# Performance work log

Measured on AMD Instinct MI355X. Metric: run time of the kernel, lower is better.

Reference implementation:

```python
import jax, jax.numpy as jnp
import numpy as np

C = 512
NH = 8
GROUPS = 32
EPS = 1e-5


def setup_inputs() -> dict:
    key = jax.random.key(0)
    ks = jax.random.split(key, 7)
    B, T, H, W = 4, 24, 32, 32
    x = jax.random.normal(ks[0], (B, C, T, H, W), dtype=jnp.float32)
    gn_w = jnp.ones((C,), jnp.float32)
    gn_b = jnp.zeros((C,), jnp.float32)
    # 1x1 Conv1d weights stored as [out_ch, in_ch] (kernel dim of size 1 dropped)
    qkv_w = jax.random.normal(ks[1], (3 * C, C), dtype=jnp.float32) / np.sqrt(C)
    qkv_b = jax.random.normal(ks[2], (3 * C,), dtype=jnp.float32) * 0.02
    proj_w = jax.random.normal(ks[3], (C, C), dtype=jnp.float32) / np.sqrt(C)
    proj_b = jax.random.normal(ks[4], (C,), dtype=jnp.float32) * 0.02
    return {"x": x, "gn_w": gn_w, "gn_b": gn_b, "qkv_w": qkv_w,
            "qkv_b": qkv_b, "proj_w": proj_w, "proj_b": proj_b}


def reference(x, gn_w, gn_b, qkv_w, qkv_b, proj_w, proj_b):
    B, Cc, T, H, W = x.shape
    hd = Cc // NH
    # [B,C,T,H,W] -> [B*H*W, C, T]
    xf = jnp.transpose(x, (0, 3, 4, 1, 2)).reshape(B * H * W, Cc, T)
    # GroupNorm over (C/G, T) per group
    xg = xf.reshape(-1, GROUPS, Cc // GROUPS, T)
    mean = xg.mean(axis=(2, 3), keepdims=True)
    var = xg.var(axis=(2, 3), keepdims=True)
    xn = ((xg - mean) * jax.lax.rsqrt(var + EPS)).reshape(-1, Cc, T)
    xn = xn * gn_w[:, None] + gn_b[:, None]
    # 1x1 conv QKV: [n, 3C, T]
    qkv = jnp.einsum('nct,dc->ndt', xn, qkv_w) + qkv_b[:, None]
    qkv = qkv.reshape(-1, 3, NH, hd, T)
    q, k, v = qkv[:, 0], qkv[:, 1], qkv[:, 2]  # each [n, h, d, T]
    scale = 1.0 / np.sqrt(hd)
    attn = jax.nn.softmax(jnp.einsum('nhdt,nhds->nhts', q, k) * scale, axis=-1)
    out = jnp.einsum('nhts,nhds->nhtd', attn, v)        # [n, h, T, d]
    out = out.transpose(0, 2, 1, 3).reshape(-1, T, Cc)   # [n, T, C]
    out = out.transpose(0, 2, 1)                         # [n, C, T]
    out = jnp.einsum('nct,dc->ndt', out, proj_w) + proj_b[:, None]
    out = out.reshape(B, H, W, Cc, T).transpose(0, 3, 4, 1, 2)
    return x + out
```

## Files before the change

### kernel.cpp

```cpp
#include <hip/hip_runtime.h>
#include <hip/hip_bf16.h>
#include <stdint.h>

#define C_    512
#define T_    24
#define HWSZ  1024
#define NN    4096
#define JTOT  98304
#define EPSV  1e-5f

typedef short short8 __attribute__((ext_vector_type(8)));
typedef short short4v __attribute__((ext_vector_type(4)));
typedef float f32x4 __attribute__((ext_vector_type(4)));
typedef float f32x2 __attribute__((ext_vector_type(2)));
typedef __bf16 bf16x2 __attribute__((ext_vector_type(2)));

typedef __attribute__((address_space(1))) const uint32_t glob_u32;
typedef __attribute__((address_space(3))) uint32_t lds_u32;

#if __has_builtin(__builtin_amdgcn_fdot2_f32_bf16)
#define HAS_DOT2 1
#else
#define HAS_DOT2 0
#endif

__device__ __forceinline__ unsigned short f2bf(float f) {
  union { float f; unsigned u; } v; v.f = f;
  unsigned r = v.u + 0x7fffu + ((v.u >> 16) & 1u);
  return (unsigned short)(r >> 16);
}
__device__ __forceinline__ float bf2f(unsigned short b) {
  union { unsigned u; float f; } v; v.u = ((unsigned)b) << 16;
  return v.f;
}
__device__ __forceinline__ float bflo(uint32_t u) {
  union { unsigned u; float f; } v; v.u = u << 16; return v.f;
}
__device__ __forceinline__ float bfhi(uint32_t u) {
  union { unsigned u; float f; } v; v.u = u & 0xffff0000u; return v.f;
}
__device__ __forceinline__ uint32_t pkbf(float a, float b) {
  return (uint32_t)f2bf(a) | ((uint32_t)f2bf(b) << 16);
}
__device__ __forceinline__ bf16x2 asbf2(uint32_t u) {
  union { uint32_t u; bf16x2 v; } c; c.u = u; return c.v;
}

__device__ __forceinline__ void gload_lds16(const void* g, void* l) {
  __builtin_amdgcn_global_load_lds((glob_u32*)g, (lds_u32*)l, 16, 0, 0);
}

__global__ void k_cvt(const float* __restrict__ qkvw, const float* __restrict__ projw,
                      unsigned short* __restrict__ qkvw_bf, unsigned short* __restrict__ projw_bf) {
  int i = blockIdx.x * 256 + threadIdx.x;
  if (i < 786432) qkvw_bf[i] = f2bf(qkvw[i]);
  if (i < 262144) projw_bf[i] = f2bf(projw[i]);
}

__global__ __launch_bounds__(256) void k_stats(const float* __restrict__ x,
                                               float* __restrict__ mean, float* __restrict__ rstd) {
  int bid = blockIdx.x;
  int g = bid & 31, hwt = (bid >> 5) & 15, b = bid >> 9;
  int tid = threadIdx.x, lane = tid & 63, grp = tid >> 6;
  int hw = hwt * 64 + lane;
  float s = 0.f, sq = 0.f;
  for (int ct = grp; ct < 384; ct += 4) {
    int c = g * 16 + ct / 24;
    int t = ct % 24;
    float v = x[((size_t)((b * 512 + c) * 24 + t) << 10) + hw];
    s += v; sq += v * v;
  }
  __shared__ float ls[4][64], lq[4][64];
  ls[grp][lane] = s; lq[grp][lane] = sq;
  __syncthreads();
  if (tid < 64) {
    float S = ls[0][tid] + ls[1][tid] + ls[2][tid] + ls[3][tid];
    float Q = lq[0][tid] + lq[1][tid] + lq[2][tid] + lq[3][tid];
    float m = S * (1.f / 384.f);
    float var = Q * (1.f / 384.f) - m * m;
    int n = b * HWSZ + hwt * 64 + tid;
    mean[n * 32 + g] = m;
    rstd[n * 32 + g] = rsqrtf(var + EPSV);
  }
}

__global__ __launch_bounds__(256) void k_norm(const float* __restrict__ x,
                                              const float* __restrict__ mean, const float* __restrict__ rstd,
                                              const float* __restrict__ gnw, const float* __restrict__ gnb,
                                              unsigned short* __restrict__ xn) {
  __shared__ unsigned short xs[64][260];
  const int bid = blockIdx.x;
  const int hwt = bid & 15;
  const int chalf = (bid >> 4) & 1;
  const int tb = bid >> 5;
  const int t = tb % 24, b = tb / 24;
  const int hw0 = hwt * 64;
  const int tid = threadIdx.x;
  const int w = tid >> 6, lane = tid & 63;

  const int cslot = w * 4 + (lane >> 4);
  const int hwr = (lane & 15) * 4;
#pragma unroll
  for (int k = 0; k < 8; ++k) {
    const int crel = k * 32 + cslot * 2;
    const int c = chalf * 256 + crel;
    const float4 v0 = *reinterpret_cast<const float4*>(
        &x[(((size_t)(b * 512 + c) * 24 + t) << 10) + hw0 + hwr]);
    const float4 v1 = *reinterpret_cast<const float4*>(
        &x[(((size_t)(b * 512 + c + 1) * 24 + t) << 10) + hw0 + hwr]);
    *reinterpret_cast<uint32_t*>(&xs[hwr + 0][crel]) = pkbf(v0.x, v1.x);
    *reinterpret_cast<uint32_t*>(&xs[hwr + 1][crel]) = pkbf(v0.y, v1.y);
    *reinterpret_cast<uint32_t*>(&xs[hwr + 2][crel]) = pkbf(v0.z, v1.z);
    *reinterpret_cast<uint32_t*>(&xs[hwr + 3][crel]) = pkbf(v0.w, v1.w);
  }

  const int crel8 = (lane & 31) * 8;
  const int c8 = chalf * 256 + crel8;
  const int g = c8 >> 4;
  float gw[8], gb[8];
#pragma unroll
  for (int i = 0; i < 8; ++i) { gw[i] = gnw[c8 + i]; gb[i] = gnb[c8 + i]; }
  float mm[8], rr[8];
#pragma unroll
  for (int p = 0; p < 8; ++p) {
    const int nrel = (p * 4 + w) * 2 + (lane >> 5);
    const int ng = b * HWSZ + hw0 + nrel;
    mm[p] = mean[ng * 32 + g];
    rr[p] = rstd[ng * 32 + g];
  }
  __syncthreads();

#pragma unroll
  for (int p = 0; p < 8; ++p) {
    const int nrel = (p * 4 + w) * 2 + (lane >> 5);
    const short4v lo = *reinterpret_cast<const short4v*>(&xs[nrel][crel8]);
    const short4v hi = *reinterpret_cast<const short4v*>(&xs[nrel][crel8 + 4]);
    float y[8];
#pragma unroll
    for (int i = 0; i < 4; ++i) {
      y[i]     = (bf2f((unsigned short)lo[i]) - mm[p]) * rr[p] * gw[i]     + gb[i];
      y[i + 4] = (bf2f((unsigned short)hi[i]) - mm[p]) * rr[p] * gw[i + 4] + gb[i + 4];
    }
    uint4 wv;
    wv.x = pkbf(y[0], y[1]);
    wv.y = pkbf(y[2], y[3]);
    wv.z = pkbf(y[4], y[5]);
    wv.w = pkbf(y[6], y[7]);
    const size_t j = (size_t)t * NN + b * HWSZ + hw0 + nrel;
    *reinterpret_cast<uint4*>(&xn[j * C_ + c8]) = wv;
  }
}

#define STAGE8(mat, half, tile, Gptr, row0)                                           \
  {                                                                                   \
    unsigned short* _l = &lds[(((tile) & 1) * 2 + (mat))][half][(w * 2) * 512];       \
    const unsigned short* _g = (Gptr) +                                               \
        (size_t)((row0) + (half) * 128 + (w * 2) * 8 + srow) * 512 +                  \
        (tile) * 64 + sslot * 8;                                                      \
    gload_lds16(_g, _l);                                                              \
    gload_lds16(_g + 8 * 512, _l + 512);                                              \
  }

__global__ __launch_bounds__(512, 2) void k_gemm8(
    const unsigned short* __restrict__ A,
    const unsigned short* __restrict__ B,
    const float* __restrict__ bias,
    uint32_t* __restrict__ outP) {
  __shared__ __attribute__((aligned(16))) unsigned short lds[4][2][8192];
  const int bid = blockIdx.x;
  const int cpx = 2304 >> 3;
  const int lid = (bid & 7) * cpx + (bid >> 3);
  const int mt = lid % 6, jt = lid / 6;
  const int m0 = mt * 256, j0 = jt * 256;
  const int tid = threadIdx.x;
  const int w = tid >> 6, lane = tid & 63;
  const int l16 = lane & 15, lqq = lane >> 4;
  const int wm = w >> 2, wn = w & 3;
  const int srow = lane >> 3;
  const int sslot = (lane & 7) ^ srow;
  const int k0off = l16 * 64 + ((lqq ^ (l16 & 7)) * 8);
  const int k1off = l16 * 64 + (((lqq + 4) ^ (l16 & 7)) * 8);

  f32x4 acc[8][4];
#pragma unroll
  for (int i = 0; i < 8; ++i)
#pragma unroll
    for (int j = 0; j < 4; ++j) acc[i][j] = {0.f, 0.f, 0.f, 0.f};

  STAGE8(0, 0, 0, A, m0); STAGE8(0, 1, 0, A, m0);
  STAGE8(1, 0, 0, B, j0); STAGE8(1, 1, 0, B, j0);
  STAGE8(0, 0, 1, A, m0); STAGE8(0, 1, 1, A, m0);
  STAGE8(1, 0, 1, B, j0);
  asm volatile("s_waitcnt vmcnt(6)" ::: "memory");
  __builtin_amdgcn_s_barrier();

  for (int t = 0; t < 8; ++t) {
    const int buf = t & 1;
    const unsigned short* Ab = &lds[buf * 2 + 0][wm][0];
    const unsigned short* Bb = &lds[buf * 2 + 1][wn >> 1][(wn & 1) * 4096];
    short8 a[8][2], bb[4][2];
#pragma unroll
    for (int rr = 0; rr < 8; ++rr) {
      a[rr][0] = *reinterpret_cast<const short8*>(Ab + rr * 1024 + k0off);
      a[rr][1] = *reinterpret_cast<const short8*>(Ab + rr * 1024 + k1off);
    }
#pragma unroll
    for (int cc = 0; cc < 2; ++cc) {
      bb[cc][0] = *reinterpret_cast<const short8*>(Bb + cc * 1024 + k0off);
      bb[cc][1] = *reinterpret_cast<const short8*>(Bb + cc * 1024 + k1off);
    }
    if (t < 7) STAGE8(1, 1, t + 1, B, j0);
    asm volatile("" ::: "memory");
    __builtin_amdgcn_s_barrier();
    asm volatile("s_waitcnt lgkmcnt(0)" ::: "memory");
    __builtin_amdgcn_sched_barrier(0);
    __builtin_amdgcn_s_setprio(1);
#pragma unroll
    for (int rr = 0; rr < 4; ++rr)
#pragma unroll
      for (int cc = 0; cc < 2; ++cc) {
        acc[rr][cc] = __builtin_amdgcn_mfma_f32_16x16x32_bf16(a[rr][0], bb[cc][0], acc[rr][cc], 0, 0, 0);
        acc[rr][cc] = __builtin_amdgcn_mfma_f32_16x16x32_bf16(a[rr][1], bb[cc][1], acc[rr][cc], 0, 0, 0);
      }
    __builtin_amdgcn_s_setprio(0);
    asm volatile("" ::: "memory");
    __builtin_amdgcn_s_barrier();
#pragma unroll
    for (int cc = 2; cc < 4; ++cc) {
      bb[cc][0] = *reinterpret_cast<const short8*>(Bb + cc * 1024 + k0off);
      bb[cc][1] = *reinterpret_cast<const short8*>(Bb + cc * 1024 + k1off);
    }
    if (t < 6) STAGE8(0, 0, t + 2, A, m0);
    asm volatile("" ::: "memory");
    __builtin_amdgcn_s_barrier();
    asm volatile("s_waitcnt lgkmcnt(0)" ::: "memory");
    __builtin_amdgcn_sched_barrier(0);
    __builtin_amdgcn_s_setprio(1);
#pragma unroll
    for (int rr = 0; rr < 4; ++rr)
#pragma unroll
      for (int cc = 2; cc < 4; ++cc) {
        acc[rr][cc] = __builtin_amdgcn_mfma_f32_16x16x32_bf16(a[rr][0], bb[cc][0], acc[rr][cc], 0, 0, 0);
        acc[rr][cc] = __builtin_amdgcn_mfma_f32_16x16x32_bf16(a[rr][1], bb[cc][1], acc[rr][cc], 0, 0, 0);
      }
    __builtin_amdgcn_s_setprio(0);
    asm volatile("" ::: "memory");
    __builtin_amdgcn_s_barrier();
    if (t < 6) STAGE8(0, 1, t + 2, A, m0);
    asm volatile("" ::: "memory");
    __builtin_amdgcn_s_barrier();
    __builtin_amdgcn_s_setprio(1);
#pragma unroll
    for (int rr = 4; rr < 8; ++rr)
#pragma unroll
      for (int cc = 0; cc < 2; ++cc) {
        acc[rr][cc] = __builtin_amdgcn_mfma_f32_16x16x32_bf16(a[rr][0], bb[cc][0], acc[rr][cc], 0, 0, 0);
        acc[rr][cc] = __builtin_amdgcn_mfma_f32_16x16x32_bf16(a[rr][1], bb[cc][1], acc[rr][cc], 0, 0, 0);
      }
    __builtin_amdgcn_s_setprio(0);
    asm volatile("" ::: "memory");
    __builtin_amdgcn_s_barrier();
    if (t < 6) STAGE8(1, 0, t + 2, B, j0);
    asm volatile("" ::: "memory");
    __builtin_amdgcn_s_barrier();
    __builtin_amdgcn_s_setprio(1);
#pragma unroll
    for (int rr = 4; rr < 8; ++rr)
#pragma unroll
      for (int cc = 2; cc < 4; ++cc) {
        acc[rr][cc] = __builtin_amdgcn_mfma_f32_16x16x32_bf16(a[rr][0], bb[cc][0], acc[rr][cc], 0, 0, 0);
        acc[rr][cc] = __builtin_amdgcn_mfma_f32_16x16x32_bf16(a[rr][1], bb[cc][1], acc[rr][cc], 0, 0, 0);
      }
    __builtin_amdgcn_s_setprio(0);
    asm volatile("" ::: "memory");
    if (t < 6) {
      asm volatile("s_waitcnt vmcnt(6)" ::: "memory");
    } else if (t == 6) {
      asm volatile("s_waitcnt vmcnt(0)" ::: "memory");
    }
    __builtin_amdgcn_s_barrier();
  }

#pragma unroll
  for (int rr = 0; rr < 8; ++rr) {
#pragma unroll
    for (int cc = 0; cc < 4; ++cc) {
      const int row = m0 + wm * 128 + rr * 16 + lqq * 4;
      const int col = j0 + wn * 64 + cc * 16 + l16;
      const int t_ = col >> 12, n = col & 4095;
      const int mat = row >> 9;
      const int hh = (row >> 6) & 7;
      const int d = row & 63;
      const int ch = d >> 3;
      const int dp = (d & 7) >> 1;
      const size_t base = (size_t)((mat * 8 + hh) * 8 + ch) * 393216;
      uint2 st;
      st.x = pkbf(acc[rr][cc][0] + bias[row], acc[rr][cc][1] + bias[row + 1]);
      st.y = pkbf(acc[rr][cc][2] + bias[row + 2], acc[rr][cc][3] + bias[row + 3]);
      *reinterpret_cast<uint2*>(&outP[base + ((size_t)t_ * 4096 + n) * 4 + dp]) = st;
    }
  }
}

__global__ __launch_bounds__(256, 3) void k_proj(
    const unsigned short* __restrict__ A,
    const unsigned short* __restrict__ B,
    const float* __restrict__ bias,
    const float* __restrict__ xres,
    float* __restrict__ outf) {
  __shared__ __attribute__((aligned(16))) unsigned short As[2][8192];
  const int bid = blockIdx.x;
  const int cpx = 3072 >> 3;
  const int lid = (bid & 7) * cpx + (bid >> 3);
  const int mt = lid & 3, jt = lid >> 2;
  const int m0 = mt * 128, j0 = jt * 128;
  const int tid = threadIdx.x;
  const int w = tid >> 6, lane = tid & 63;
  const int l16 = lane & 15, lqq = lane >> 4;
  const int wm = w >> 1, wn = w & 1;
  const int srow8 = lane >> 3;
  const int sslot = (lane & 7) ^ srow8;
  const int k0off = l16 * 64 + ((lqq ^ (l16 & 7)) * 8);
  const int k1off = l16 * 64 + (((lqq + 4) ^ (l16 & 7)) * 8);

  f32x4 acc[4][4];
#pragma unroll
  for (int i = 0; i < 4; ++i)
#pragma unroll
    for (int j = 0; j < 4; ++j) acc[i][j] = {0.f, 0.f, 0.f, 0.f};

#define PSTAGE(buf, tile)                                                             \
  {                                                                                   \
    _Pragma("unroll")                                                                 \
    for (int m_ = 0; m_ < 4; ++m_) {                                                  \
      unsigned short* _l = &As[buf][m_ * 2048 + w * 512];                             \
      const unsigned short* _g = A +                                                  \
          (size_t)(m0 + m_ * 32 + w * 8 + srow8) * 512 + (tile) * 64 + sslot * 8;     \
      gload_lds16(_g, _l);                                                            \
    }                                                                                 \
  }

#define LOADB(dst, tt)                                                                \
  {                                                                                   \
    _Pragma("unroll")                                                                 \
    for (int cc = 0; cc < 4; ++cc) {                                                  \
      const int jj_ = j0 + wn * 64 + cc * 16 + l16;                                   \
      _Pragma("unroll")                                                               \
      for (int ks = 0; ks < 2; ++ks)                                                  \
        dst[cc][ks] = *reinterpret_cast<const short8*>(                               \
            &B[((size_t)((tt) * 8 + ks * 4 + lqq) * JTOT + jj_) * 8]);                \
    }                                                                                 \
  }

#define PSTEP(t, CUR, NXT)                                                            \
  {                                                                                   \
    if ((t) < 7) { PSTAGE(((t) + 1) & 1, (t) + 1); LOADB(NXT, (t) + 1); }             \
    const unsigned short* Ab = &As[(t) & 1][(wm * 64) * 64];                          \
    _Pragma("unroll")                                                                 \
    for (int rr = 0; rr < 4; ++rr) {                                                  \
      short8 a0 = *reinterpret_cast<const short8*>(Ab + rr * 1024 + k0off);           \
      short8 a1 = *reinterpret_cast<const short8*>(Ab + rr * 1024 + k1off);           \
      _Pragma("unroll")                                                               \
      for (int cc = 0; cc < 4; ++cc) {                                                \
        acc[rr][cc] = __builtin_amdgcn_mfma_f32_16x16x32_bf16(a0, CUR[cc][0], acc[rr][cc], 0, 0, 0); \
        acc[rr][cc] = __builtin_amdgcn_mfma_f32_16x16x32_bf16(a1, CUR[cc][1], acc[rr][cc], 0, 0, 0); \
      }                                                                               \
    }                                                                                 \
    __syncthreads();                                                                  \
  }

  short8 bbA[4][2], bbB[4][2];
  PSTAGE(0, 0);
  LOADB(bbA, 0);
  __syncthreads();

  PSTEP(0, bbA, bbB);
  PSTEP(1, bbB, bbA);
  PSTEP(2, bbA, bbB);
  PSTEP(3, bbB, bbA);
  PSTEP(4, bbA, bbB);
  PSTEP(5, bbB, bbA);
  PSTEP(6, bbA, bbB);
  PSTEP(7, bbB, bbA);

#pragma unroll
  for (int mi = 0; mi < 4; ++mi) {
#pragma unroll
    for (int ni = 0; ni < 4; ++ni) {
      const int dbase = m0 + wm * 64 + mi * 16 + lqq * 4;
      const int jj = j0 + wn * 64 + ni * 16 + l16;
      const int t_ = jj >> 12, n = jj & 4095;
      const int b_ = n >> 10, hw = n & 1023;
#pragma unroll
      for (int r = 0; r < 4; ++r) {
        size_t o = (((size_t)(b_ * 512 + dbase + r) * 24 + t_) << 10) + hw;
        outf[o] = xres[o] + acc[mi][ni][r] + bias[dbase + r];
      }
    }
  }
}

__global__ __launch_bounds__(512) void k_attn(const uint32_t* __restrict__ qkvP,
                                              unsigned short* __restrict__ aoC) {
  __shared__ uint4 kq[2][1536];
  const int ntile = blockIdx.x, h = blockIdx.y;
  const int n0 = ntile * 64;
  const int tid = threadIdx.x;
  const int lane = tid & 63, slot = tid >> 6;
  const int t0 = slot * 3;
  const int BLK = 393216;
  const size_t bQ = (size_t)((0 * 8 + h) * 8) * BLK;
  const size_t bK = (size_t)((1 * 8 + h) * 8) * BLK;
  const size_t bV = (size_t)((2 * 8 + h) * 8) * BLK;
  const int ub = tid & 448;

#define STAGE_M(cbase, dstbuf)                                                        \
  {                                                                                   \
    _Pragma("unroll")                                                                 \
    for (int p = 0; p < 3; ++p) {                                                     \
      const int u = p * 512 + tid;                                                    \
      gload_lds16(qkvP + (cbase) + ((size_t)(u >> 6) * 4096 + n0 + (u & 63)) * 4,     \
                  (void*)(&kq[dstbuf][p * 512 + ub]));                                \
    }                                                                                 \
  }

#define STAGE_QK(c_)                                                                  \
  {                                                                                   \
    STAGE_M(bK + (size_t)(c_) * BLK, 0);                                              \
    STAGE_M(bQ + (size_t)(c_) * BLK, 1);                                              \
  }

#define STAGE_V(c_) { STAGE_M(bV + (size_t)(c_) * BLK, 0); }

  float S[3][24];
#pragma unroll
  for (int a = 0; a < 3; ++a)
#pragma unroll
    for (int s = 0; s < 24; ++s) S[a][s] = 0.f;

  STAGE_QK(0);
  __syncthreads();
  for (int c = 0; c < 8; ++c) {
    uint4 qv[3];
#pragma unroll
    for (int a = 0; a < 3; ++a) qv[a] = kq[1][(t0 + a) * 64 + lane];
#if !HAS_DOT2
    float qf[3][8];
#pragma unroll
    for (int a = 0; a < 3; ++a) {
      qf[a][0] = bflo(qv[a].x); qf[a][1] = bfhi(qv[a].x);
      qf[a][2] = bflo(qv[a].y); qf[a][3] = bfhi(qv[a].y);
      qf[a][4] = bflo(qv[a].z); qf[a][5] = bfhi(qv[a].z);
      qf[a][6] = bflo(qv[a].w); qf[a][7] = bfhi(qv[a].w);
    }
#endif
#pragma unroll
    for (int s = 0; s < 24; ++s) {
      const uint4 kk = kq[0][s * 64 + lane];
#if HAS_DOT2
#pragma unroll
      for (int a = 0; a < 3; ++a) {
        S[a][s] = __builtin_amdgcn_fdot2_f32_bf16(asbf2(qv[a].x), asbf2(kk.x), S[a][s], false);
        S[a][s] = __builtin_amdgcn_fdot2_f32_bf16(asbf2(qv[a].y), asbf2(kk.y), S[a][s], false);
        S[a][s] = __builtin_amdgcn_fdot2_f32_bf16(asbf2(qv[a].z), asbf2(kk.z), S[a][s], false);
        S[a][s] = __builtin_amdgcn_fdot2_f32_bf16(asbf2(qv[a].w), asbf2(kk.w), S[a][s], false);
      }
#else
      const float k0 = bflo(kk.x), k1 = bfhi(kk.x), k2 = bflo(kk.y), k3 = bfhi(kk.y);
      const float k4 = bflo(kk.z), k5 = bfhi(kk.z), k6 = bflo(kk.w), k7 = bfhi(kk.w);
#pragma unroll
      for (int a = 0; a < 3; ++a) {
        S[a][s] = fmaf(qf[a][0], k0, S[a][s]); S[a][s] = fmaf(qf[a][1], k1, S[a][s]);
        S[a][s] = fmaf(qf[a][2], k2, S[a][s]); S[a][s] = fmaf(qf[a][3], k3, S[a][s]);
        S[a][s] = fmaf(qf[a][4], k4, S[a][s]); S[a][s] = fmaf(qf[a][5], k5, S[a][s]);
        S[a][s] = fmaf(qf[a][6], k6, S[a][s]); S[a][s] = fmaf(qf[a][7], k7, S[a][s]);
      }
#endif
    }
    __syncthreads();
    if (c < 7) {
      STAGE_QK(c + 1);
      __syncthreads();
    }
  }

#pragma unroll
  for (int a = 0; a < 3; ++a) {
    float mx = S[a][0];
#pragma unroll
    for (int s = 1; s < 24; ++s) mx = fmaxf(mx, S[a][s]);
    float sum = 0.f;
#pragma unroll
    for (int s = 0; s < 24; ++s) {
      float e = __expf((S[a][s] - mx) * 0.125f);
      S[a][s] = e; sum += e;
    }
    float inv = 1.f / sum;
#pragma unroll
    for (int s = 0; s < 24; ++s) S[a][s] *= inv;
  }

  STAGE_V(0);
  __syncthreads();
  for (int c = 0; c < 8; ++c) {
    f32x2 o2[3][4];
#pragma unroll
    for (int a = 0; a < 3; ++a)
#pragma unroll
      for (int dp = 0; dp < 4; ++dp) o2[a][dp] = {0.f, 0.f};
#pragma unroll
    for (int s = 0; s < 24; ++s) {
      const uint4 vv = kq[0][s * 64 + lane];
      f32x2 v0, v1, v2, v3;
      v0.x = bflo(vv.x); v0.y = bfhi(vv.x);
      v1.x = bflo(vv.y); v1.y = bfhi(vv.y);
      v2.x = bflo(vv.z); v2.y = bfhi(vv.z);
      v3.x = bflo(vv.w); v3.y = bfhi(vv.w);
#pragma unroll
      for (int a = 0; a < 3; ++a) {
        o2[a][0] += S[a][s] * v0;
        o2[a][1] += S[a][s] * v1;
        o2[a][2] += S[a][s] * v2;
        o2[a][3] += S[a][s] * v3;
      }
    }
#pragma unroll
    for (int a = 0; a < 3; ++a) {
      uint4 wv;
      wv.x = pkbf(o2[a][0].x, o2[a][0].y);
      wv.y = pkbf(o2[a][1].x, o2[a][1].y);
      wv.z = pkbf(o2[a][2].x, o2[a][2].y);
      wv.w = pkbf(o2[a][3].x, o2[a][3].y);
      const size_t unit = (size_t)(h * 8 + c) * JTOT + (size_t)(t0 + a) * NN + n0 + lane;
      *reinterpret_cast<uint4*>(&aoC[unit * 8]) = wv;
    }
    __syncthreads();
    if (c < 7) {
      STAGE_V(c + 1);
      __syncthreads();
    }
  }
}

extern "C" void kernel_launch(void* const* d_in, const int* in_sizes, int n_in,
                              void* d_out, int out_size, void* d_ws, size_t ws_size,
                              hipStream_t stream) {
  (void)in_sizes; (void)n_in; (void)out_size; (void)ws_size;
  const float* x     = (const float*)d_in[0];
  const float* gnw   = (const float*)d_in[1];
  const float* gnb   = (const float*)d_in[2];
  const float* qkvw  = (const float*)d_in[3];
  const float* qkvb  = (const float*)d_in[4];
  const float* projw = (const float*)d_in[5];
  const float* projb = (const float*)d_in[6];
  float* out = (float*)d_out;
  char* ws = (char*)d_ws;

  unsigned short* qkvw_bf = (unsigned short*)(ws);
  unsigned short* projw_bf = (unsigned short*)(ws + 1572864);
  float* mean = (float*)(ws + 2097152);
  float* rstd = (float*)(ws + 2621440);
  unsigned short* xn  = (unsigned short*)(ws + 3145728);
  uint32_t* qkvP = (uint32_t*)(ws + 3145728 + 100663296);

  k_cvt<<<dim3(3072), dim3(256), 0, stream>>>(qkvw, projw, qkvw_bf, projw_bf);
  k_stats<<<dim3(2048), dim3(256), 0, stream>>>(x, mean, rstd);
  k_norm<<<dim3(3072), dim3(256), 0, stream>>>(x, mean, rstd, gnw, gnb, xn);
  k_gemm8<<<dim3(2304), dim3(512), 0, stream>>>(qkvw_bf, xn, qkvb, qkvP);
  k_attn<<<dim3(64, 8), dim3(512), 0, stream>>>(qkvP, xn);
  k_proj<<<dim3(3072), dim3(256), 0, stream>>>(projw_bf, xn, projb, x, out);
}
```

Before: 513.2 us.

## Double-buffer K/V staging in attention kernel and load Q directly from global

The attention kernel now stages K (and then V) chunks into two alternating LDS buffers, issuing the next chunk's async global-to-LDS load before computing on the current one. One barrier with an explicit vmcnt wait replaces the pair of syncthreads per chunk. Q is read straight from global memory into registers instead of through LDS, which frees the second buffer for double-buffering. The aim is to hide global load latency behind the dot-product work, in exchange for uncached per-thread Q loads and hand-written waitcnt/barrier ordering that must stay correct.

New measurement: 517.4 us. About the same (+0.8%).

```diff
diff --git a/kernel.cpp b/kernel.cpp
--- a/kernel.cpp
+++ b/kernel.cpp
@@ -402,7 +402,7 @@
 
 __global__ __launch_bounds__(512) void k_attn(const uint32_t* __restrict__ qkvP,
                                               unsigned short* __restrict__ aoC) {
-  __shared__ uint4 kq[2][1536];
+  __shared__ uint4 kb[2][1536];
   const int ntile = blockIdx.x, h = blockIdx.y;
   const int n0 = ntile * 64;
   const int tid = threadIdx.x;
@@ -420,30 +420,31 @@
     for (int p = 0; p < 3; ++p) {                                                     \
       const int u = p * 512 + tid;                                                    \
       gload_lds16(qkvP + (cbase) + ((size_t)(u >> 6) * 4096 + n0 + (u & 63)) * 4,     \
-                  (void*)(&kq[dstbuf][p * 512 + ub]));                                \
+                  (void*)(&kb[dstbuf][p * 512 + ub]));                                \
     }                                                                                 \
   }
 
-#define STAGE_QK(c_)                                                                  \
-  {                                                                                   \
-    STAGE_M(bK + (size_t)(c_) * BLK, 0);                                              \
-    STAGE_M(bQ + (size_t)(c_) * BLK, 1);                                              \
-  }
-
-#define STAGE_V(c_) { STAGE_M(bV + (size_t)(c_) * BLK, 0); }
-
   float S[3][24];
 #pragma unroll
   for (int a = 0; a < 3; ++a)
 #pragma unroll
     for (int s = 0; s < 24; ++s) S[a][s] = 0.f;
 
-  STAGE_QK(0);
-  __syncthreads();
+  STAGE_M(bK, 0);
+  asm volatile("s_waitcnt vmcnt(0)" ::: "memory");
+  __builtin_amdgcn_s_barrier();
+
   for (int c = 0; c < 8; ++c) {
+    if (c < 7) {
+      STAGE_M(bK + (size_t)(c + 1) * BLK, (c + 1) & 1);
+    } else {
+      STAGE_M(bV, 0);
+    }
     uint4 qv[3];
 #pragma unroll
-    for (int a = 0; a < 3; ++a) qv[a] = kq[1][(t0 + a) * 64 + lane];
+    for (int a = 0; a < 3; ++a)
+      qv[a] = *reinterpret_cast<const uint4*>(
+          qkvP + bQ + (size_t)c * BLK + ((size_t)(t0 + a) * 4096 + n0 + lane) * 4);
 #if !HAS_DOT2
     float qf[3][8];
 #pragma unroll
@@ -454,9 +455,10 @@
       qf[a][6] = bflo(qv[a].w); qf[a][7] = bfhi(qv[a].w);
     }
 #endif
+    const uint4* kbuf = kb[c & 1];
 #pragma unroll
     for (int s = 0; s < 24; ++s) {
-      const uint4 kk = kq[0][s * 64 + lane];
+      const uint4 kk = kbuf[s * 64 + lane];
 #if HAS_DOT2
 #pragma unroll
       for (int a = 0; a < 3; ++a) {
@@ -477,11 +479,8 @@
       }
 #endif
     }
-    __syncthreads();
-    if (c < 7) {
-      STAGE_QK(c + 1);
-      __syncthreads();
-    }
+    asm volatile("s_waitcnt vmcnt(0)" ::: "memory");
+    __builtin_amdgcn_s_barrier();
   }
 
 #pragma unroll
@@ -500,17 +499,17 @@
     for (int s = 0; s < 24; ++s) S[a][s] *= inv;
   }
 
-  STAGE_V(0);
-  __syncthreads();
   for (int c = 0; c < 8; ++c) {
+    if (c < 7) STAGE_M(bV + (size_t)(c + 1) * BLK, (c + 1) & 1);
     f32x2 o2[3][4];
 #pragma unroll
     for (int a = 0; a < 3; ++a)
 #pragma unroll
       for (int dp = 0; dp < 4; ++dp) o2[a][dp] = {0.f, 0.f};
+    const uint4* vbuf = kb[c & 1];
 #pragma unroll
     for (int s = 0; s < 24; ++s) {
-      const uint4 vv = kq[0][s * 64 + lane];
+      const uint4 vv = vbuf[s * 64 + lane];
       f32x2 v0, v1, v2, v3;
       v0.x = bflo(vv.x); v0.y = bfhi(vv.x);
       v1.x = bflo(vv.y); v1.y = bfhi(vv.y);
@@ -534,11 +533,8 @@
       const size_t unit = (size_t)(h * 8 + c) * JTOT + (size_t)(t0 + a) * NN + n0 + lane;
       *reinterpret_cast<uint4*>(&aoC[unit * 8]) = wv;
     }
-    __syncthreads();
-    if (c < 7) {
-      STAGE_V(c + 1);
-      __syncthreads();
-    }
+    asm volatile("s_waitcnt vmcnt(0)" ::: "memory");
+    __builtin_amdgcn_s_barrier();
   }
 }
 
```
